# Kernel optimization log

Hardware: AMD Instinct MI355X
Metric: run time of the kernel (lower is better)

## Reference

```python
import jax, jax.numpy as jnp
import numpy as np

# Directable[TL_table[i]] for i = 0..7: (dx, dy) with dx=horizontal shift, dy=vertical shift
# dx=+1 -> shift right (zero-fill col 0), dx=-1 -> shift left; dy=+1 -> shift down, dy=-1 -> shift up.
DIRS = [(1, 1), (0, 1), (-1, 1), (1, 0), (-1, 0), (1, -1), (0, -1), (-1, -1)]


def _shift(img, dx, dy):
    # img: [B, H, W]; zero-padded shift equivalent to bmm with the sparse translation matrices
    if dx == 1:
        img = jnp.pad(img[..., :-1], ((0, 0), (0, 0), (1, 0)))
    elif dx == -1:
        img = jnp.pad(img[..., 1:], ((0, 0), (0, 0), (0, 1)))
    if dy == 1:
        img = jnp.pad(img[:, :-1, :], ((0, 0), (1, 0), (0, 0)))
    elif dy == -1:
        img = jnp.pad(img[:, 1:, :], ((0, 0), (0, 1), (0, 0)))
    return img


def _bce(p, t):
    # torch F.binary_cross_entropy clamps log terms at -100
    logp = jnp.maximum(jnp.log(p), -100.0)
    log1mp = jnp.maximum(jnp.log(1.0 - p), -100.0)
    return -jnp.mean(t * logp + (1.0 - t) * log1mp)


def setup_inputs() -> dict:
    key = jax.random.key(0)
    k1, k2, k3 = jax.random.split(key, 3)
    B, C, H, W = 16, 8, 512, 512
    c_map = jax.random.normal(k1, (B, C, H, W), dtype=jnp.float32)
    target = jax.random.randint(k2, (B, 1, H, W), 0, 2, dtype=jnp.int32)
    con_target = jax.random.randint(k3, (B, C, H, W), 0, 2, dtype=jnp.int32)
    return {"c_map": c_map, "target": target, "con_target": con_target}


def reference(c_map, target, con_target):
    target = target.astype(jnp.float32)        # [B,1,H,W]
    con_target = con_target.astype(jnp.float32)  # [B,8,H,W]

    p = jax.nn.sigmoid(c_map)  # [B,8,H,W]

    # Bilateral voting: shifted[i] = shift(p[:, 7-i]) in direction DIRS[i]
    shifted = jnp.stack(
        [_shift(p[:, 7 - i], dx, dy) for i, (dx, dy) in enumerate(DIRS)], axis=1
    )  # [B,8,H,W]
    vote_out = p * shifted                       # [B,8,H,W] (== bimap.squeeze(1))
    final_pred = jnp.max(vote_out, axis=1, keepdims=True)  # [B,1,H,W]

    # dice loss (sums over dims (1,2) of the 4D tensors, as in the original)
    smooth = 0.001
    i_sum = jnp.sum(target, axis=(1, 2))
    j_sum = jnp.sum(final_pred, axis=(1, 2))
    inter = jnp.sum(target * final_pred, axis=(1, 2))
    loss_dice = jnp.mean(1.0 - (2.0 * inter + smooth) / (i_sum + j_sum + smooth))

    # edge (decouple) loss
    sum_conn = jnp.sum(con_target, axis=1)  # [B,H,W]
    edge = ((sum_conn < 8) & (sum_conn > 0)).astype(p.dtype)
    pred_min = jnp.min(vote_out, axis=1) * edge
    decouple_loss = _bce(pred_min, jnp.zeros_like(pred_min))

    bce_loss = _bce(final_pred, target)
    conmap_l = _bce(p, con_target)
    bimap_l = _bce(vote_out, con_target)

    return 0.8 * conmap_l + decouple_loss + 0.2 * bimap_l + bce_loss + loss_dice
```

## Files before the change

kernel.cpp:

```cpp
#include <hip/hip_runtime.h>

namespace {
constexpr int Bn = 16, Cn = 8, Hn = 512, Wn = 512;
constexpr int HW  = Hn * Wn;
constexpr int CHW = Cn * HW;
constexpr int NCOL = Bn * Wn;
constexpr int NBLK = 8 * 8 * 16;

__device__ __forceinline__ float fsigmoid(float x) {
    return __builtin_amdgcn_rcpf(1.0f + __expf(-x));
}
}


__global__ __launch_bounds__(256) void bicon_main(
    const float* __restrict__ c_map,
    const int*   __restrict__ target,
    const int*   __restrict__ con_target,
    float* __restrict__ col_i,
    float* __restrict__ col_j,
    float* __restrict__ col_x,
    double* __restrict__ bscal)
{
    constexpr int DX[8] = {1, 0, -1, 1, -1, 1, 0, -1};
    constexpr int DY[8] = {1, 1, 1, 0, 0, -1, -1, -1};

    const int tx = threadIdx.x;
    const int ty = threadIdx.y;
    const int b  = blockIdx.z;
    const int w  = (blockIdx.x << 6) + tx;
    const int h0 = blockIdx.y << 6;

    const float* cm = c_map      + (size_t)b * CHW;
    const int*   ct = con_target + (size_t)b * CHW;
    const int*   tg = target     + (size_t)b * HW;

    float s_con = 0.0f, s_bi = 0.0f, s_bce = 0.0f, s_dec = 0.0f;
    float ci = 0.0f, cj = 0.0f, cx = 0.0f;

    for (int hh = ty; hh < 64; hh += 4) {
        const int h    = h0 + hh;
        const int base = h * Wn + w;

        float p[8], nb[8];
        int   t8[8];
#pragma unroll
        for (int c = 0; c < 8; ++c) {
            const int idx = c * HW + base;
            p[c]  = fsigmoid(cm[idx]);
            t8[c] = ct[idx];
            const int hn = h + DY[c];
            const int wn = w + DX[c];
            float nv = 0.0f;
            if ((unsigned)hn < (unsigned)Hn && (unsigned)wn < (unsigned)Wn) {
                nv = fsigmoid(cm[idx + DY[c] * Wn + DX[c]]);
            }
            nb[c] = nv;
        }
        const int t = tg[base];

        float vmax = -1.0f, vmin = 2.0f;
        int   sumc = 0;
        float it_con = 0.0f, it_bi = 0.0f;
#pragma unroll
        for (int i = 0; i < 8; ++i) {
            const float v = p[i] * nb[7 - i];
            vmax  = fmaxf(vmax, v);
            vmin  = fminf(vmin, v);
            sumc += t8[i];
            it_con += fmaxf(__logf(t8[i] ? p[i] : 1.0f - p[i]), -100.0f);
            it_bi  += fmaxf(__logf(t8[i] ? v    : 1.0f - v),    -100.0f);
        }
        s_con += it_con;
        s_bi  += it_bi;
        s_bce += fmaxf(__logf(t ? vmax : 1.0f - vmax), -100.0f);
        if ((sumc > 0) & (sumc < 8)) {
            s_dec += fmaxf(__logf(1.0f - vmin), -100.0f);
        }

        ci += (float)t;
        cj += vmax;
        cx += t ? vmax : 0.0f;
    }

    __shared__ float colred[3][4][64];
    colred[0][ty][tx] = ci;
    colred[1][ty][tx] = cj;
    colred[2][ty][tx] = cx;

#pragma unroll
    for (int off = 32; off > 0; off >>= 1) {
        s_con += __shfl_down(s_con, off);
        s_bi  += __shfl_down(s_bi,  off);
        s_bce += __shfl_down(s_bce, off);
        s_dec += __shfl_down(s_dec, off);
    }
    __shared__ float wred[4][4];
    if (tx == 0) {
        wred[ty][0] = s_con;
        wred[ty][1] = s_bi;
        wred[ty][2] = s_bce;
        wred[ty][3] = s_dec;
    }
    __syncthreads();

    if (ty == 0) {
        const float a0 = colred[0][0][tx] + colred[0][1][tx] + colred[0][2][tx] + colred[0][3][tx];
        const float a1 = colred[1][0][tx] + colred[1][1][tx] + colred[1][2][tx] + colred[1][3][tx];
        const float a2 = colred[2][0][tx] + colred[2][1][tx] + colred[2][2][tx] + colred[2][3][tx];
        const int col = b * Wn + w;
        atomicAdd(&col_i[col], a0);
        atomicAdd(&col_j[col], a1);
        atomicAdd(&col_x[col], a2);
    }
    if (ty == 1 && tx < 4) {
        const int bid = (blockIdx.z * 8 + (int)blockIdx.y) * 8 + (int)blockIdx.x;
        bscal[bid * 4 + tx] =
            (double)(wred[0][tx] + wred[1][tx] + wred[2][tx] + wred[3][tx]);
    }
}

__global__ __launch_bounds__(256) void bicon_finish(
    const float* __restrict__ col_i,
    const float* __restrict__ col_j,
    const float* __restrict__ col_x,
    const double* __restrict__ bscal,
    float* __restrict__ out)
{
    const int tid = threadIdx.x;

    double dsum = 0.0;
    for (int idx = tid; idx < NCOL; idx += 256) {
        const float fi = col_i[idx], fj = col_j[idx], fx = col_x[idx];
        dsum += (double)(1.0f - (2.0f * fx + 0.001f) / (fi + fj + 0.001f));
    }
    double s0 = 0.0, s1 = 0.0, s2 = 0.0, s3 = 0.0;
    for (int s = tid; s < NBLK; s += 256) {
        s0 += bscal[s * 4 + 0];
        s1 += bscal[s * 4 + 1];
        s2 += bscal[s * 4 + 2];
        s3 += bscal[s * 4 + 3];
    }
#pragma unroll
    for (int off = 32; off > 0; off >>= 1) {
        dsum += __shfl_down(dsum, off);
        s0   += __shfl_down(s0, off);
        s1   += __shfl_down(s1, off);
        s2   += __shfl_down(s2, off);
        s3   += __shfl_down(s3, off);
    }
    __shared__ double red[5][4];
    const int wv = tid >> 6, ln = tid & 63;
    if (ln == 0) {
        red[0][wv] = dsum; red[1][wv] = s0; red[2][wv] = s1;
        red[3][wv] = s2;   red[4][wv] = s3;
    }
    __syncthreads();
    if (tid == 0) {
        const double dice   =  (red[0][0] + red[0][1] + red[0][2] + red[0][3]) / 8192.0;
        const double conmap = -(red[1][0] + red[1][1] + red[1][2] + red[1][3]) / 33554432.0;
        const double bimap  = -(red[2][0] + red[2][1] + red[2][2] + red[2][3]) / 33554432.0;
        const double bce    = -(red[3][0] + red[3][1] + red[3][2] + red[3][3]) / 4194304.0;
        const double dec    = -(red[4][0] + red[4][1] + red[4][2] + red[4][3]) / 4194304.0;
        out[0] = (float)(0.8 * conmap + dec + 0.2 * bimap + bce + dice);
    }
}

extern "C" void kernel_launch(void* const* d_in, const int* in_sizes, int n_in,
                              void* d_out, int out_size, void* d_ws, size_t ws_size,
                              hipStream_t stream) {
    const float* c_map      = (const float*)d_in[0];
    const int*   target     = (const int*)d_in[1];
    const int*   con_target = (const int*)d_in[2];
    float* out = (float*)d_out;

    char* ws = (char*)d_ws;
    float*  col_i = (float*)ws;
    float*  col_j = col_i + NCOL;
    float*  col_x = col_j + NCOL;
    double* bscal = (double*)(ws + 3 * NCOL * sizeof(float));

    hipMemsetAsync(d_ws, 0, 3 * NCOL * sizeof(float), stream);

    dim3 grid(Wn / 64, Hn / 64, Bn);
    dim3 block(64, 4);
    bicon_main<<<grid, block, 0, stream>>>(c_map, target, con_target,
                                           col_i, col_j, col_x, bscal);
    bicon_finish<<<1, 256, 0, stream>>>(col_i, col_j, col_x, bscal, out);
}
```

Measured before the change: 337.8 us.

## Vectorize per-thread 8-pixel strips with shuffle-based horizontal neighbors and parallel finish

Each thread now handles eight consecutive pixels of a full-width row, using float4/int4 loads. Horizontal neighbor values come from in-register shifts plus wave shuffles rather than separate unaligned loads. Each neighbor row's sigmoid is computed once per channel pair. The conmap BCE is computed algebraically from log(1+e^-x), and con_target bits are packed into masks with popcount giving the edge test. The finish kernel is spread over 32 blocks with an atomic add into the output. Register pressure rises and the result now depends on atomic float accumulation order.

```diff
diff --git a/kernel.cpp b/kernel.cpp
--- a/kernel.cpp
+++ b/kernel.cpp
@@ -5,11 +5,12 @@
 constexpr int HW  = Hn * Wn;
 constexpr int CHW = Cn * HW;
 constexpr int NCOL = Bn * Wn;
-constexpr int NBLK = 8 * 8 * 16;
-
-__device__ __forceinline__ float fsigmoid(float x) {
-    return __builtin_amdgcn_rcpf(1.0f + __expf(-x));
-}
+constexpr int ROWS = 8;
+constexpr int GY   = Hn / ROWS;
+constexpr int NBLK = GY * Bn;
+constexpr int FBLK = 32;
+
+__device__ __forceinline__ float frcp(float x) { return __builtin_amdgcn_rcpf(x); }
 }
 
 
@@ -17,76 +18,145 @@
     const float* __restrict__ c_map,
     const int*   __restrict__ target,
     const int*   __restrict__ con_target,
-    float* __restrict__ col_i,
-    float* __restrict__ col_j,
-    float* __restrict__ col_x,
+    float* __restrict__ col_i, float* __restrict__ col_j, float* __restrict__ col_x,
     double* __restrict__ bscal)
 {
-    constexpr int DX[8] = {1, 0, -1, 1, -1, 1, 0, -1};
-    constexpr int DY[8] = {1, 1, 1, 0, 0, -1, -1, -1};
-
     const int tx = threadIdx.x;
     const int ty = threadIdx.y;
-    const int b  = blockIdx.z;
-    const int w  = (blockIdx.x << 6) + tx;
-    const int h0 = blockIdx.y << 6;
+    const int b  = blockIdx.y;
+    const int h0 = blockIdx.x * ROWS;
+    const int wq = tx << 3;
 
     const float* cm = c_map      + (size_t)b * CHW;
     const int*   ct = con_target + (size_t)b * CHW;
     const int*   tg = target     + (size_t)b * HW;
 
-    float s_con = 0.0f, s_bi = 0.0f, s_bce = 0.0f, s_dec = 0.0f;
-    float ci = 0.0f, cj = 0.0f, cx = 0.0f;
-
-    for (int hh = ty; hh < 64; hh += 4) {
-        const int h    = h0 + hh;
-        const int base = h * Wn + w;
-
-        float p[8], nb[8];
-        int   t8[8];
+    float s_con = 0.f, s_bi = 0.f, s_bce = 0.f, s_dec = 0.f;
+    float ci[8], cj[8], cx[8];
+#pragma unroll
+    for (int k = 0; k < 8; ++k) { ci[k] = cj[k] = cx[k] = 0.f; }
+
+#pragma unroll
+    for (int it = 0; it < ROWS / 4; ++it) {
+        const int h    = h0 + ty + it * 4;
+        const int base = h * Wn + wq;
+
+        int tp[8] = {0, 0, 0, 0, 0, 0, 0, 0};
 #pragma unroll
         for (int c = 0; c < 8; ++c) {
-            const int idx = c * HW + base;
-            p[c]  = fsigmoid(cm[idx]);
-            t8[c] = ct[idx];
-            const int hn = h + DY[c];
-            const int wn = w + DX[c];
-            float nv = 0.0f;
-            if ((unsigned)hn < (unsigned)Hn && (unsigned)wn < (unsigned)Wn) {
-                nv = fsigmoid(cm[idx + DY[c] * Wn + DX[c]]);
+            const int4 u0 = *(const int4*)(ct + c * HW + base);
+            const int4 u1 = *(const int4*)(ct + c * HW + base + 4);
+            tp[0] |= u0.x << c; tp[1] |= u0.y << c; tp[2] |= u0.z << c; tp[3] |= u0.w << c;
+            tp[4] |= u1.x << c; tp[5] |= u1.y << c; tp[6] |= u1.z << c; tp[7] |= u1.w << c;
+        }
+
+        float vmax[8], vmin[8];
+#pragma unroll
+        for (int k = 0; k < 8; ++k) { vmax[k] = 0.f; vmin[k] = 2.f; }
+
+        auto center = [&](int c, float s[8]) {
+            const float* p = cm + c * HW + base;
+            const float4 v0 = *(const float4*)p;
+            const float4 v1 = *(const float4*)(p + 4);
+            const float xs[8] = {v0.x, v0.y, v0.z, v0.w, v1.x, v1.y, v1.z, v1.w};
+#pragma unroll
+            for (int k = 0; k < 8; ++k) {
+                const float e = __expf(-xs[k]);
+                const float d = 1.f + e;
+                s[k] = frcp(d);
+                const float logd = __logf(d);
+                const float term = ((tp[k] >> c) & 1) ? -logd : (-xs[k] - logd);
+                s_con += fmaxf(term, -100.f);
             }
-            nb[c] = nv;
-        }
-        const int t = tg[base];
-
-        float vmax = -1.0f, vmin = 2.0f;
-        int   sumc = 0;
-        float it_con = 0.0f, it_bi = 0.0f;
-#pragma unroll
-        for (int i = 0; i < 8; ++i) {
-            const float v = p[i] * nb[7 - i];
-            vmax  = fmaxf(vmax, v);
-            vmin  = fminf(vmin, v);
-            sumc += t8[i];
-            it_con += fmaxf(__logf(t8[i] ? p[i] : 1.0f - p[i]), -100.0f);
-            it_bi  += fmaxf(__logf(t8[i] ? v    : 1.0f - v),    -100.0f);
-        }
-        s_con += it_con;
-        s_bi  += it_bi;
-        s_bce += fmaxf(__logf(t ? vmax : 1.0f - vmax), -100.0f);
-        if ((sumc > 0) & (sumc < 8)) {
-            s_dec += fmaxf(__logf(1.0f - vmin), -100.0f);
-        }
-
-        ci += (float)t;
-        cj += vmax;
-        cx += t ? vmax : 0.0f;
-    }
-
-    __shared__ float colred[3][4][64];
-    colred[0][ty][tx] = ci;
-    colred[1][ty][tx] = cj;
-    colred[2][ty][tx] = cx;
+        };
+
+        auto nbrrow = [&](int c, int dy, float sp[8]) {
+            const int hn = h + dy;
+            if ((unsigned)hn < (unsigned)Hn) {
+                const float* p = cm + c * HW + hn * Wn + wq;
+                const float4 v0 = *(const float4*)p;
+                const float4 v1 = *(const float4*)(p + 4);
+                const float xs[8] = {v0.x, v0.y, v0.z, v0.w, v1.x, v1.y, v1.z, v1.w};
+#pragma unroll
+                for (int k = 0; k < 8; ++k) sp[k] = frcp(1.f + __expf(-xs[k]));
+            } else {
+#pragma unroll
+                for (int k = 0; k < 8; ++k) sp[k] = 0.f;
+            }
+        };
+
+        auto shplus = [&](const float sp[8], float n[8]) {
+#pragma unroll
+            for (int k = 0; k < 7; ++k) n[k] = sp[k + 1];
+            const float t = __shfl_down(sp[0], 1);
+            n[7] = (tx == 63) ? 0.f : t;
+        };
+        auto shminus = [&](const float sp[8], float n[8]) {
+#pragma unroll
+            for (int k = 7; k > 0; --k) n[k] = sp[k - 1];
+            const float t = __shfl_up(sp[7], 1);
+            n[0] = (tx == 0) ? 0.f : t;
+        };
+
+        auto vote = [&](int i, const float si[8], const float nn[8]) {
+#pragma unroll
+            for (int k = 0; k < 8; ++k) {
+                const float v = si[k] * nn[k];
+                vmax[k] = fmaxf(vmax[k], v);
+                vmin[k] = fminf(vmin[k], v);
+                const float arg = ((tp[k] >> i) & 1) ? v : (1.f - v);
+                s_bi += fmaxf(__logf(arg), -100.f);
+            }
+        };
+
+        {
+            float sa[8], sb[8], sp[8], n[8];
+            center(0, sa); center(7, sb);
+            nbrrow(0, +1, sp); shplus(sp, n);  vote(7, sb, n);
+            nbrrow(7, -1, sp); shminus(sp, n); vote(0, sa, n);
+        }
+        {
+            float sa[8], sb[8], sp[8];
+            center(1, sa); center(6, sb);
+            nbrrow(1, +1, sp); vote(6, sb, sp);
+            nbrrow(6, -1, sp); vote(1, sa, sp);
+        }
+        {
+            float sa[8], sb[8], sp[8], n[8];
+            center(2, sa); center(5, sb);
+            nbrrow(2, +1, sp); shminus(sp, n); vote(5, sb, n);
+            nbrrow(5, -1, sp); shplus(sp, n);  vote(2, sa, n);
+        }
+        {
+            float sa[8], sb[8], n[8];
+            center(3, sa); center(4, sb);
+            shplus(sa, n);  vote(4, sb, n);
+            shminus(sb, n); vote(3, sa, n);
+        }
+
+        const int4 t0 = *(const int4*)(tg + base);
+        const int4 t1 = *(const int4*)(tg + base + 4);
+        const int tk[8] = {t0.x, t0.y, t0.z, t0.w, t1.x, t1.y, t1.z, t1.w};
+#pragma unroll
+        for (int k = 0; k < 8; ++k) {
+            const float fm = vmax[k];
+            s_bce += fmaxf(__logf(tk[k] ? fm : 1.f - fm), -100.f);
+            const int sc = __popc(tp[k]);
+            const float le = fmaxf(__logf(1.f - vmin[k]), -100.f);
+            s_dec += (sc > 0 && sc < 8) ? le : 0.f;
+            ci[k] += (float)tk[k];
+            cj[k] += fm;
+            cx[k] += tk[k] ? fm : 0.f;
+        }
+    }
+
+    __shared__ float cred[3][4][512];
+#pragma unroll
+    for (int k = 0; k < 8; ++k) {
+        cred[0][ty][wq + k] = ci[k];
+        cred[1][ty][wq + k] = cj[k];
+        cred[2][ty][wq + k] = cx[k];
+    }
 
 #pragma unroll
     for (int off = 32; off > 0; off >>= 1) {
@@ -97,26 +167,24 @@
     }
     __shared__ float wred[4][4];
     if (tx == 0) {
-        wred[ty][0] = s_con;
-        wred[ty][1] = s_bi;
-        wred[ty][2] = s_bce;
-        wred[ty][3] = s_dec;
+        wred[ty][0] = s_con; wred[ty][1] = s_bi;
+        wred[ty][2] = s_bce; wred[ty][3] = s_dec;
     }
     __syncthreads();
 
-    if (ty == 0) {
-        const float a0 = colred[0][0][tx] + colred[0][1][tx] + colred[0][2][tx] + colred[0][3][tx];
-        const float a1 = colred[1][0][tx] + colred[1][1][tx] + colred[1][2][tx] + colred[1][3][tx];
-        const float a2 = colred[2][0][tx] + colred[2][1][tx] + colred[2][2][tx] + colred[2][3][tx];
-        const int col = b * Wn + w;
-        atomicAdd(&col_i[col], a0);
-        atomicAdd(&col_j[col], a1);
-        atomicAdd(&col_x[col], a2);
-    }
-    if (ty == 1 && tx < 4) {
-        const int bid = (blockIdx.z * 8 + (int)blockIdx.y) * 8 + (int)blockIdx.x;
-        bscal[bid * 4 + tx] =
-            (double)(wred[0][tx] + wred[1][tx] + wred[2][tx] + wred[3][tx]);
+    const int tid = ty * 64 + tx;
+#pragma unroll
+    for (int j = tid; j < 512; j += 256) {
+        const float a0 = cred[0][0][j] + cred[0][1][j] + cred[0][2][j] + cred[0][3][j];
+        const float a1 = cred[1][0][j] + cred[1][1][j] + cred[1][2][j] + cred[1][3][j];
+        const float a2 = cred[2][0][j] + cred[2][1][j] + cred[2][2][j] + cred[2][3][j];
+        atomicAdd(&col_i[b * Wn + j], a0);
+        atomicAdd(&col_j[b * Wn + j], a1);
+        atomicAdd(&col_x[b * Wn + j], a2);
+    }
+    if (tid < 4) {
+        bscal[((size_t)blockIdx.y * GY + blockIdx.x) * 4 + tid] =
+            (double)(wred[0][tid] + wred[1][tid] + wred[2][tid] + wred[3][tid]);
     }
 }
 
@@ -128,42 +196,27 @@
     float* __restrict__ out)
 {
     const int tid = threadIdx.x;
-
-    double dsum = 0.0;
-    for (int idx = tid; idx < NCOL; idx += 256) {
-        const float fi = col_i[idx], fj = col_j[idx], fx = col_x[idx];
-        dsum += (double)(1.0f - (2.0f * fx + 0.001f) / (fi + fj + 0.001f));
-    }
-    double s0 = 0.0, s1 = 0.0, s2 = 0.0, s3 = 0.0;
-    for (int s = tid; s < NBLK; s += 256) {
-        s0 += bscal[s * 4 + 0];
-        s1 += bscal[s * 4 + 1];
-        s2 += bscal[s * 4 + 2];
-        s3 += bscal[s * 4 + 3];
-    }
-#pragma unroll
-    for (int off = 32; off > 0; off >>= 1) {
-        dsum += __shfl_down(dsum, off);
-        s0   += __shfl_down(s0, off);
-        s1   += __shfl_down(s1, off);
-        s2   += __shfl_down(s2, off);
-        s3   += __shfl_down(s3, off);
-    }
-    __shared__ double red[5][4];
-    const int wv = tid >> 6, ln = tid & 63;
-    if (ln == 0) {
-        red[0][wv] = dsum; red[1][wv] = s0; red[2][wv] = s1;
-        red[3][wv] = s2;   red[4][wv] = s3;
-    }
+    const int col = blockIdx.x * 256 + tid;
+
+    double part;
+    {
+        const float fi = col_i[col], fj = col_j[col], fx = col_x[col];
+        part = (1.0 - (2.0 * (double)fx + 0.001) /
+                      ((double)fi + (double)fj + 0.001)) / 8192.0;
+    }
+    if (tid < 32) {
+        const int s = blockIdx.x * 32 + tid;
+        const double c0 = bscal[s * 4 + 0], c1 = bscal[s * 4 + 1];
+        const double c2 = bscal[s * 4 + 2], c3 = bscal[s * 4 + 3];
+        part += -0.8 * c0 / 33554432.0 - 0.2 * c1 / 33554432.0
+                - c2 / 4194304.0 - c3 / 4194304.0;
+    }
+#pragma unroll
+    for (int off = 32; off > 0; off >>= 1) part += __shfl_down(part, off);
+    __shared__ double red[4];
+    if ((tid & 63) == 0) red[tid >> 6] = part;
     __syncthreads();
-    if (tid == 0) {
-        const double dice   =  (red[0][0] + red[0][1] + red[0][2] + red[0][3]) / 8192.0;
-        const double conmap = -(red[1][0] + red[1][1] + red[1][2] + red[1][3]) / 33554432.0;
-        const double bimap  = -(red[2][0] + red[2][1] + red[2][2] + red[2][3]) / 33554432.0;
-        const double bce    = -(red[3][0] + red[3][1] + red[3][2] + red[3][3]) / 4194304.0;
-        const double dec    = -(red[4][0] + red[4][1] + red[4][2] + red[4][3]) / 4194304.0;
-        out[0] = (float)(0.8 * conmap + dec + 0.2 * bimap + bce + dice);
-    }
+    if (tid == 0) atomicAdd(out, (float)(red[0] + red[1] + red[2] + red[3]));
 }
 
 extern "C" void kernel_launch(void* const* d_in, const int* in_sizes, int n_in,
@@ -181,10 +234,11 @@
     double* bscal = (double*)(ws + 3 * NCOL * sizeof(float));
 
     hipMemsetAsync(d_ws, 0, 3 * NCOL * sizeof(float), stream);
-
-    dim3 grid(Wn / 64, Hn / 64, Bn);
+    hipMemsetAsync(d_out, 0, sizeof(float), stream);
+
+    dim3 grid(GY, Bn);
     dim3 block(64, 4);
     bicon_main<<<grid, block, 0, stream>>>(c_map, target, con_target,
                                            col_i, col_j, col_x, bscal);
-    bicon_finish<<<1, 256, 0, stream>>>(col_i, col_j, col_x, bscal, out);
-}
+    bicon_finish<<<FBLK, 256, 0, stream>>>(col_i, col_j, col_x, bscal, out);
+}
```

After: 349.3 us. 3.4% more time.
